# Optimization experiments

Measured on AMD Instinct MI355X. Metric: run time of the kernel, lower is better.

Reference implementation:

```python
import jax, jax.numpy as jnp
import numpy as np

N_X, N_M, E, D_IN, D_OUT = 200000, 50000, 600000, 128, 128
BN_EPS = 1e-5


def setup_inputs() -> dict:
    key = jax.random.key(0)
    ks = jax.random.split(key, 12)
    s = 0.02
    x_metrical = jax.random.normal(ks[0], (N_M, D_IN), dtype=jnp.float32)
    x = jax.random.normal(ks[1], (N_X, D_IN), dtype=jnp.float32)
    src = jax.random.randint(ks[2], (E,), 0, N_X)   # indexes x (note nodes)
    dst = jax.random.randint(ks[3], (E,), 0, N_M)   # indexes x_metrical
    edge_index = jnp.stack([src, dst], axis=0)
    batch = jnp.zeros((N_M,), dtype=jnp.int64 if jax.config.jax_enable_x64 else jnp.int32)
    return {
        "x_metrical": x_metrical,
        "x": x,
        "edge_index": edge_index,
        "batch": batch,
        "W_neigh": jax.random.normal(ks[4], (D_IN, D_IN), dtype=jnp.float32) * s,
        "b_neigh": jnp.zeros((D_IN,), dtype=jnp.float32),
        "W_l": jax.random.normal(ks[5], (D_IN, D_IN), dtype=jnp.float32) * s,  # SAGEConv lin_l (neighbors)
        "b_l": jnp.zeros((D_IN,), dtype=jnp.float32),
        "W_r": jax.random.normal(ks[6], (D_IN, D_IN), dtype=jnp.float32) * s,  # SAGEConv lin_r (root, no bias)
        "W_out": jax.random.normal(ks[7], (D_OUT, 3 * D_IN), dtype=jnp.float32) * s,
        "b_out": jnp.zeros((D_OUT,), dtype=jnp.float32),
        "gamma": jnp.ones((D_OUT,), dtype=jnp.float32),
        "beta": jnp.zeros((D_OUT,), dtype=jnp.float32),
    }


def reference(x_metrical, x, edge_index, batch, W_neigh, b_neigh, W_l, b_l, W_r,
              W_out, b_out, gamma, beta):
    n_m = x_metrical.shape[0]
    n_x = x.shape[0]
    src, dst = edge_index[0], edge_index[1]

    # neigh linear on note features, scatter-add onto metrical nodes
    h_neigh = x @ W_neigh.T + b_neigh                          # [N_x, D]
    h_scatter = jax.ops.segment_sum(h_neigh[src], dst, num_segments=n_m)  # [N_m, D]

    # SAGEConv(aggr='add') over the chain seq_index (batch all-equal branch):
    # edge i -> i+1, so sum-aggregation = shift x_metrical down by one row.
    agg = jnp.concatenate(
        [jnp.zeros((1, x_metrical.shape[1]), dtype=x_metrical.dtype), x_metrical[:-1]],
        axis=0)
    h_seq = agg @ W_l.T + b_l + x_metrical @ W_r.T             # [N_m, D]

    # concat + output linear (activation = Identity)
    h = jnp.concatenate([h_scatter, x_metrical, h_seq], axis=1)  # [N_m, 3D]
    h = h @ W_out.T + b_out                                      # [N_m, D_out]

    # BatchNorm1d (training-mode batch stats, biased variance); dropout = identity (eval)
    mean = jnp.mean(h, axis=0)
    var = jnp.mean((h - mean) ** 2, axis=0)
    h = (h - mean) * jax.lax.rsqrt(var + BN_EPS) * gamma + beta

    # final scatter-add back onto note nodes
    out = jax.ops.segment_sum(h[dst], src, num_segments=n_x)     # [N_x, D_out]
    return out
```

## Files before the change

kernel.cpp:

```cpp
#include <hip/hip_runtime.h>

#define D_IN 128
#define BN_EPS 1e-5f
#define BIN_SHIFT 8
#define MAXBIN 1024

typedef __attribute__((ext_vector_type(8))) __bf16 bf16x8;
typedef __attribute__((ext_vector_type(8))) unsigned short ushort8;
typedef __attribute__((ext_vector_type(4))) float f32x4;
typedef unsigned short ushort_t;

__device__ inline ushort_t f2bf(float x) {
    union { float f; unsigned u; } c; c.f = x;
    unsigned r = (c.u + 0x7fffu + ((c.u >> 16) & 1u)) >> 16;
    return (ushort_t)r;
}
__device__ inline float bf2f(ushort_t x) {
    union { unsigned u; float f; } c; c.u = ((unsigned)x) << 16;
    return c.f;
}
__device__ inline float lof(unsigned v) {
    union { unsigned u; float f; } c; c.u = v << 16;
    return c.f;
}
__device__ inline float hif(unsigned v) {
    union { unsigned u; float f; } c; c.u = v & 0xffff0000u;
    return c.f;
}

__global__ void combine_weights_k(const float* __restrict__ Wn, const float* __restrict__ bn,
                                  const float* __restrict__ Wl, const float* __restrict__ bl,
                                  const float* __restrict__ Wr, const float* __restrict__ Wo,
                                  const float* __restrict__ bo,
                                  ushort_t* __restrict__ Wb, float* __restrict__ c1,
                                  float* __restrict__ c0,
                                  int* __restrict__ binCnt,
                                  const float* __restrict__ xm, ushort_t* __restrict__ xmb,
                                  int n8m) {
    int b = blockIdx.x;
    int j = threadIdx.x;
    if (b < 384) {
        int term = b >> 7;
        int k = b & 127;
        float acc = 0.f;
        if (term == 0) {
            for (int t = 0; t < 128; ++t) acc += Wo[j * 384 + t] * Wn[t * 128 + k];
        } else if (term == 1) {
            acc = Wo[j * 384 + 128 + k];
            for (int t = 0; t < 128; ++t) acc += Wo[j * 384 + 256 + t] * Wr[t * 128 + k];
        } else {
            for (int t = 0; t < 128; ++t) acc += Wo[j * 384 + 256 + t] * Wl[t * 128 + k];
        }
        Wb[term * 16384 + j * 128 + k] = f2bf(acc);
    } else if (b == 384) {
        float a1 = 0.f, a0 = bo[j];
        for (int t = 0; t < 128; ++t) {
            a1 += Wo[j * 384 + t] * bn[t];
            a0 += Wo[j * 384 + 256 + t] * bl[t];
        }
        c1[j] = a1;
        c0[j] = a0;
    } else if (b == 385) {
        for (int i = j; i < MAXBIN; i += 128) binCnt[i] = 0;
    } else {
        int i = (b - 386) * 128 + j;
        if (i < n8m) {
            float4 f0 = ((const float4*)xm)[i * 2];
            float4 f1 = ((const float4*)xm)[i * 2 + 1];
            ushort8 o;
            o[0] = f2bf(f0.x); o[1] = f2bf(f0.y); o[2] = f2bf(f0.z); o[3] = f2bf(f0.w);
            o[4] = f2bf(f1.x); o[5] = f2bf(f1.y); o[6] = f2bf(f1.z); o[7] = f2bf(f1.w);
            ((ushort8*)xmb)[i] = o;
        }
    }
}


__global__ __launch_bounds__(256) void bin_hist_k(const int* __restrict__ src,
                                                  const int* __restrict__ dst,
                                                  int* __restrict__ binCnt,
                                                  int nE, int nM, int nBin) {
    __shared__ int h[MAXBIN];
    int t = threadIdx.x;
    for (int i = t; i < nBin; i += 256) h[i] = 0;
    __syncthreads();
    int total = 2 * nE;
    int per = (total + gridDim.x - 1) / gridDim.x;
    int lo = blockIdx.x * per, hi = min(lo + per, total);
    for (int i = lo + t; i < hi; i += 256) {
        int key = (i < nE) ? dst[i] : (nM + src[i - nE]);
        atomicAdd(&h[key >> BIN_SHIFT], 1);
    }
    __syncthreads();
    for (int i = t; i < nBin; i += 256) {
        int v = h[i];
        if (v) atomicAdd(&binCnt[i], v);
    }
}

__global__ __launch_bounds__(1024) void bin_scan_k(const int* __restrict__ binCnt,
                                                   int* __restrict__ binBase,
                                                   int* __restrict__ binCursor,
                                                   int* __restrict__ offs,
                                                   int nBin, int nTot, int total2E) {
    __shared__ int sc[1024];
    int t = threadIdx.x;
    int v = (t < nBin) ? binCnt[t] : 0;
    sc[t] = v;
    __syncthreads();
    for (int off = 1; off < 1024; off <<= 1) {
        int a = (t >= off) ? sc[t - off] : 0;
        __syncthreads();
        sc[t] += a;
        __syncthreads();
    }
    int excl = sc[t] - v;
    if (t <= nBin) binBase[t] = excl;
    if (t < nBin) binCursor[t] = excl;
    if (t == nBin) offs[nTot] = total2E;
}

__global__ __launch_bounds__(256) void bin_scatter_k(const int* __restrict__ src,
                                                     const int* __restrict__ dst,
                                                     int* __restrict__ binCursor,
                                                     unsigned* __restrict__ binned,
                                                     int nE, int nM, int nBin) {
    __shared__ int h[MAXBIN];
    __shared__ int base[MAXBIN];
    int t = threadIdx.x;
    for (int i = t; i < nBin; i += 256) h[i] = 0;
    __syncthreads();
    int total = 2 * nE;
    int per = (total + gridDim.x - 1) / gridDim.x;
    int lo = blockIdx.x * per, hi = min(lo + per, total);
    for (int i = lo + t; i < hi; i += 256) {
        int key = (i < nE) ? dst[i] : (nM + src[i - nE]);
        atomicAdd(&h[key >> BIN_SHIFT], 1);
    }
    __syncthreads();
    for (int i = t; i < nBin; i += 256) {
        int c = h[i];
        base[i] = c ? atomicAdd(&binCursor[i], c) : 0;
        h[i] = 0;
    }
    __syncthreads();
    for (int i = lo + t; i < hi; i += 256) {
        int key, val;
        if (i < nE) { key = dst[i]; val = src[i]; }
        else        { key = nM + src[i - nE]; val = dst[i - nE]; }
        int b = key >> BIN_SHIFT;
        int p = base[b] + atomicAdd(&h[b], 1);
        binned[p] = ((unsigned)(key & ((1 << BIN_SHIFT) - 1)) << 20) | (unsigned)val;
    }
}

__global__ __launch_bounds__(256) void bucket_sort_k(const unsigned* __restrict__ binned,
                                                     const int* __restrict__ binBase,
                                                     int* __restrict__ offs,
                                                     int* __restrict__ list, int nTot) {
    __shared__ int hist[256];
    __shared__ int sc[256];
    __shared__ int cur[256];
    int b = blockIdx.x;
    int base = binBase[b], end = binBase[b + 1];
    int n = end - base;
    int t = threadIdx.x;
    hist[t] = 0;
    __syncthreads();
    for (int i = t; i < n; i += 256) atomicAdd(&hist[binned[base + i] >> 20], 1);
    __syncthreads();
    int v = hist[t];
    sc[t] = v;
    __syncthreads();
    for (int off = 1; off < 256; off <<= 1) {
        int a = (t >= off) ? sc[t - off] : 0;
        __syncthreads();
        sc[t] += a;
        __syncthreads();
    }
    int excl = sc[t] - v;
    int bucket = (b << BIN_SHIFT) + t;
    if (bucket < nTot) offs[bucket] = base + excl;
    cur[t] = excl;
    __syncthreads();
    for (int i = t; i < n; i += 256) {
        unsigned p = binned[base + i];
        int lb = p >> 20;
        int pos = atomicAdd(&cur[lb], 1);
        list[base + pos] = (int)(p & 0xFFFFFu);
    }
}


__global__ __launch_bounds__(256) void gather_xs_k(const float4* __restrict__ x4,
                                                   const int* __restrict__ offs,
                                                   const int* __restrict__ list,
                                                   uint2* __restrict__ XS4, int nM) {
    int m = blockIdx.x * 8 + (threadIdx.x >> 5);
    if (m >= nM) return;
    int l = threadIdx.x & 31;
    int s = offs[m], e = offs[m + 1];
    float a0 = 0.f, a1 = 0.f, a2 = 0.f, a3 = 0.f;
    for (int s0 = s; s0 < e; s0 += 32) {
        int cnt = min(e - s0, 32);
        int r = (l < cnt) ? list[s0 + l] : 0;
        for (int i0 = 0; i0 < cnt; i0 += 8) {
            float4 v[8];
#pragma unroll
            for (int j = 0; j < 8; ++j) {
                int idx = i0 + j;
                int cl = idx < cnt ? idx : cnt - 1;
                int rr = __shfl(r, cl, 32);
                v[j] = x4[(size_t)rr * 32 + l];
            }
#pragma unroll
            for (int j = 0; j < 8; ++j) {
                if (i0 + j < cnt) {
                    a0 += v[j].x; a1 += v[j].y; a2 += v[j].z; a3 += v[j].w;
                }
            }
        }
    }
    uint2 o;
    o.x = (unsigned)f2bf(a0) | ((unsigned)f2bf(a1) << 16);
    o.y = (unsigned)f2bf(a2) | ((unsigned)f2bf(a3) << 16);
    XS4[(size_t)m * 32 + l] = o;
}

__global__ __launch_bounds__(256) void gemm_h_k(const ushort_t* __restrict__ XSb,
                                                const ushort_t* __restrict__ XMb,
                                                const ushort_t* __restrict__ Wb,
                                                const float* __restrict__ c1,
                                                const float* __restrict__ c0,
                                                const int* __restrict__ off,
                                                ushort_t* __restrict__ Hb,
                                                float* __restrict__ partS,
                                                float* __restrict__ partQ, int nM) {
    __shared__ float lds_s[4][128];
    __shared__ float lds_q[4][128];
    int wave = threadIdx.x >> 6, lane = threadIdx.x & 63;
    int m0 = blockIdx.x * 64 + wave * 16;
    int rl = lane & 15, kg = lane >> 4;
    f32x4 acc[8];
#pragma unroll
    for (int jt = 0; jt < 8; ++jt) acc[jt] = (f32x4){0.f, 0.f, 0.f, 0.f};
    int arow = m0 + rl;
    bool wave_live = (m0 < nM);
    if (wave_live) {
#pragma unroll
        for (int term = 0; term < 3; ++term) {
            const ushort_t* xp = (term == 0) ? XSb : XMb;
            int r2 = (term == 2) ? (arow - 1) : arow;
            bool valid = (r2 >= 0) && (arow < nM);
            const ushort_t* rp = xp + (size_t)r2 * D_IN + kg * 8;
            const ushort_t* wbase = Wb + term * 16384 + rl * 128 + kg * 8;
            bf16x8 a[4];
#pragma unroll
            for (int kc = 0; kc < 4; ++kc) {
                if (valid) {
                    a[kc] = *reinterpret_cast<const bf16x8*>(rp + kc * 32);
                } else {
#pragma unroll
                    for (int i = 0; i < 8; ++i) a[kc][i] = (__bf16)0.f;
                }
            }
#pragma unroll
            for (int kc = 0; kc < 4; ++kc) {
                bf16x8 bfr[8];
#pragma unroll
                for (int jt = 0; jt < 8; ++jt)
                    bfr[jt] = *reinterpret_cast<const bf16x8*>(wbase + jt * 2048 + kc * 32);
#pragma unroll
                for (int jt = 0; jt < 8; ++jt)
                    acc[jt] = __builtin_amdgcn_mfma_f32_16x16x32_bf16(a[kc], bfr[jt], acc[jt], 0, 0, 0);
            }
        }
    }
    float ssum[8], sq[8];
#pragma unroll
    for (int jt = 0; jt < 8; ++jt) { ssum[jt] = 0.f; sq[jt] = 0.f; }
    if (wave_live) {
        float cc1[8], cc0[8];
#pragma unroll
        for (int jt = 0; jt < 8; ++jt) { cc1[jt] = c1[jt * 16 + rl]; cc0[jt] = c0[jt * 16 + rl]; }
#pragma unroll
        for (int r = 0; r < 4; ++r) {
            int rowd = m0 + kg * 4 + r;
            if (rowd < nM) {
                float degv = (float)(off[rowd + 1] - off[rowd]);
                ushort_t* hp = Hb + (size_t)rowd * D_IN;
#pragma unroll
                for (int jt = 0; jt < 8; ++jt) {
                    float hv = acc[jt][r] + degv * cc1[jt] + cc0[jt];
                    hp[jt * 16 + rl] = f2bf(hv);
                    ssum[jt] += hv;
                    sq[jt] += hv * hv;
                }
            }
        }
    }
#pragma unroll
    for (int jt = 0; jt < 8; ++jt) {
        ssum[jt] += __shfl_xor(ssum[jt], 16, 64);
        ssum[jt] += __shfl_xor(ssum[jt], 32, 64);
        sq[jt]   += __shfl_xor(sq[jt], 16, 64);
        sq[jt]   += __shfl_xor(sq[jt], 32, 64);
    }
    if (lane < 16) {
#pragma unroll
        for (int jt = 0; jt < 8; ++jt) {
            lds_s[wave][jt * 16 + rl] = ssum[jt];
            lds_q[wave][jt * 16 + rl] = sq[jt];
        }
    }
    __syncthreads();
    if (threadIdx.x < 128) {
        int col = threadIdx.x;
        float s = lds_s[0][col] + lds_s[1][col] + lds_s[2][col] + lds_s[3][col];
        float q = lds_q[0][col] + lds_q[1][col] + lds_q[2][col] + lds_q[3][col];
        partS[(size_t)blockIdx.x * 128 + col] = s;
        partQ[(size_t)blockIdx.x * 128 + col] = q;
    }
}

__global__ __launch_bounds__(1024) void bn_reduce_k(const float* __restrict__ partS,
                                                    const float* __restrict__ partQ,
                                                    float* __restrict__ bnsum,
                                                    float* __restrict__ bnsq, int nB) {
    __shared__ float ls[8][128], lq[8][128];
    int col = threadIdx.x & 127, seg = threadIdx.x >> 7;
    float s = 0.f, q = 0.f;
    for (int b = seg; b < nB; b += 8) {
        s += partS[(size_t)b * 128 + col];
        q += partQ[(size_t)b * 128 + col];
    }
    ls[seg][col] = s;
    lq[seg][col] = q;
    __syncthreads();
    if (threadIdx.x < 128) {
        float S = 0.f, Q = 0.f;
#pragma unroll
        for (int i = 0; i < 8; ++i) { S += ls[i][col]; Q += lq[i][col]; }
        bnsum[col] = S;
        bnsq[col] = Q;
    }
}

__global__ __launch_bounds__(256) void gather_out_k(const uint2* __restrict__ H4,
                                                    const int* __restrict__ offs2,
                                                    const int* __restrict__ list,
                                                    const float* __restrict__ bnsum,
                                                    const float* __restrict__ bnsq,
                                                    const float* __restrict__ gamma,
                                                    const float* __restrict__ beta,
                                                    float* __restrict__ out,
                                                    int nX, int nM) {
    int n = blockIdx.x * 8 + (threadIdx.x >> 5);
    if (n >= nX) return;
    int l = threadIdx.x & 31;
    int s = offs2[n], e = offs2[n + 1];
    float a0 = 0.f, a1 = 0.f, a2 = 0.f, a3 = 0.f;
    for (int s0 = s; s0 < e; s0 += 32) {
        int cnt = min(e - s0, 32);
        int r = (l < cnt) ? list[s0 + l] : 0;
        for (int i0 = 0; i0 < cnt; i0 += 4) {
            uint2 v[4];
#pragma unroll
            for (int j = 0; j < 4; ++j) {
                int idx = i0 + j;
                int cl = idx < cnt ? idx : cnt - 1;
                int rr = __shfl(r, cl, 32);
                v[j] = H4[(size_t)rr * 32 + l];
            }
#pragma unroll
            for (int j = 0; j < 4; ++j) {
                if (i0 + j < cnt) {
                    a0 += lof(v[j].x); a1 += hif(v[j].x);
                    a2 += lof(v[j].y); a3 += hif(v[j].y);
                }
            }
        }
    }
    float4 s1 = ((const float4*)bnsum)[l];
    float4 s2 = ((const float4*)bnsq)[l];
    float4 g  = ((const float4*)gamma)[l];
    float4 be = ((const float4*)beta)[l];
    float inv = 1.0f / (float)nM;
    float cnt = (float)(e - s);
    f32x4 o;
    {
        float mean = s1.x * inv, var = s2.x * inv - mean * mean;
        float sc = g.x * rsqrtf(var + BN_EPS);
        o.x = sc * a0 + cnt * (be.x - mean * sc);
    }
    {
        float mean = s1.y * inv, var = s2.y * inv - mean * mean;
        float sc = g.y * rsqrtf(var + BN_EPS);
        o.y = sc * a1 + cnt * (be.y - mean * sc);
    }
    {
        float mean = s1.z * inv, var = s2.z * inv - mean * mean;
        float sc = g.z * rsqrtf(var + BN_EPS);
        o.z = sc * a2 + cnt * (be.z - mean * sc);
    }
    {
        float mean = s1.w * inv, var = s2.w * inv - mean * mean;
        float sc = g.w * rsqrtf(var + BN_EPS);
        o.w = sc * a3 + cnt * (be.w - mean * sc);
    }
    __builtin_nontemporal_store(o, (f32x4*)(out + (size_t)n * 128 + l * 4));
}

extern "C" void kernel_launch(void* const* d_in, const int* in_sizes, int n_in,
                              void* d_out, int out_size, void* d_ws, size_t ws_size,
                              hipStream_t stream) {
    const float* x_metrical = (const float*)d_in[0];
    const float* x          = (const float*)d_in[1];
    const int*   edge       = (const int*)d_in[2];
    const float* Wn    = (const float*)d_in[4];
    const float* bn    = (const float*)d_in[5];
    const float* Wl    = (const float*)d_in[6];
    const float* bl    = (const float*)d_in[7];
    const float* Wr    = (const float*)d_in[8];
    const float* Wo    = (const float*)d_in[9];
    const float* bo    = (const float*)d_in[10];
    const float* gamma = (const float*)d_in[11];
    const float* beta  = (const float*)d_in[12];
    float* out = (float*)d_out;

    int nM = in_sizes[0] / D_IN;
    int nX = in_sizes[1] / D_IN;
    int nE = in_sizes[2] / 2;
    int nTot = nM + nX;
    int nBin = (nTot + 255) >> BIN_SHIFT;
    int nBlkGemm = (nM + 63) / 64;
    const int* src = edge;
    const int* dst = edge + nE;

    char* ws = (char*)d_ws;
    size_t o = 0;
    auto alloc = [&](size_t bytes) -> void* {
        void* p = ws + o;
        o = (o + bytes + 255) & ~(size_t)255;
        return p;
    };
    ushort_t* Wb        = (ushort_t*)alloc((size_t)3 * 128 * 128 * 2);
    float*    c1        = (float*)alloc(512);
    float*    c0        = (float*)alloc(512);
    float*    bnsum     = (float*)alloc(512);
    float*    bnsq      = (float*)alloc(512);
    int*      binCnt    = (int*)alloc(4096);
    int*      binBase   = (int*)alloc(4104);
    int*      binCursor = (int*)alloc(4096);
    float*    partS     = (float*)alloc((size_t)nBlkGemm * 128 * 4);
    float*    partQ     = (float*)alloc((size_t)nBlkGemm * 128 * 4);
    int*      offs      = (int*)alloc(((size_t)nTot + 1) * 4);
    int*      list      = (int*)alloc((size_t)2 * nE * 4);
    size_t unionSz = (size_t)2 * nE * 4;
    size_t xsSz = (size_t)nM * D_IN * 2;
    char* uregion = (char*)alloc(unionSz > xsSz ? unionSz : xsSz);
    unsigned* binned = (unsigned*)uregion;
    ushort_t* XSb    = (ushort_t*)uregion;
    ushort_t* xmb    = (ushort_t*)alloc((size_t)nM * D_IN * 2);
    ushort_t* Hb     = (ushort_t*)alloc((size_t)nM * D_IN * 2);

    int n8m = nM * D_IN / 8;
    int nBlkComb = 386 + (n8m + 127) / 128;
    combine_weights_k<<<nBlkComb, 128, 0, stream>>>(Wn, bn, Wl, bl, Wr, Wo, bo, Wb, c1, c0,
                                                    binCnt, x_metrical, xmb, n8m);
    bin_hist_k<<<256, 256, 0, stream>>>(src, dst, binCnt, nE, nM, nBin);
    bin_scan_k<<<1, 1024, 0, stream>>>(binCnt, binBase, binCursor, offs, nBin, nTot, 2 * nE);
    bin_scatter_k<<<256, 256, 0, stream>>>(src, dst, binCursor, binned, nE, nM, nBin);
    bucket_sort_k<<<nBin, 256, 0, stream>>>(binned, binBase, offs, list, nTot);
    gather_xs_k<<<(nM + 7) / 8, 256, 0, stream>>>((const float4*)x, offs, list,
                                                  (uint2*)XSb, nM);
    gemm_h_k<<<nBlkGemm, 256, 0, stream>>>(XSb, xmb, Wb, c1, c0, offs, Hb,
                                           partS, partQ, nM);
    bn_reduce_k<<<1, 1024, 0, stream>>>(partS, partQ, bnsum, bnsq, nBlkGemm);
    gather_out_k<<<(nX + 7) / 8, 256, 0, stream>>>((const uint2*)Hb, offs + nM, list,
                                                   bnsum, bnsq, gamma, beta,
                                                   out, nX, nM);
}
```

Before: 232.8 us.

## Fuse histogram into preprocessing kernel and gather from bf16 copy of x

The edge-key histogram now runs inside the preprocessing kernel as per-block partial histograms, which bin_scan sums. This removes the separate histogram launch and the global atomics, and drops the binCnt zeroing dependency. The preprocessing kernel also converts all of x (200k x 128) to bf16, so the random-access gather reads 8 bytes per lane instead of 16. The cost is a full extra read and write pass over x (about 100 MB of traffic) and a bin_scan that loops over 512 partial rows. It also rounds x to bf16 before summation, which changes precision.

```diff
diff --git a/kernel.cpp b/kernel.cpp
--- a/kernel.cpp
+++ b/kernel.cpp
@@ -4,6 +4,7 @@
 #define BN_EPS 1e-5f
 #define BIN_SHIFT 8
 #define MAXBIN 1024
+#define NHB 512
 
 typedef __attribute__((ext_vector_type(8))) __bf16 bf16x8;
 typedef __attribute__((ext_vector_type(8))) unsigned short ushort8;
@@ -15,10 +16,6 @@
     unsigned r = (c.u + 0x7fffu + ((c.u >> 16) & 1u)) >> 16;
     return (ushort_t)r;
 }
-__device__ inline float bf2f(ushort_t x) {
-    union { unsigned u; float f; } c; c.u = ((unsigned)x) << 16;
-    return c.f;
-}
 __device__ inline float lof(unsigned v) {
     union { unsigned u; float f; } c; c.u = v << 16;
     return c.f;
@@ -28,20 +25,36 @@
     return c.f;
 }
 
-__global__ void combine_weights_k(const float* __restrict__ Wn, const float* __restrict__ bn,
-                                  const float* __restrict__ Wl, const float* __restrict__ bl,
-                                  const float* __restrict__ Wr, const float* __restrict__ Wo,
-                                  const float* __restrict__ bo,
-                                  ushort_t* __restrict__ Wb, float* __restrict__ c1,
-                                  float* __restrict__ c0,
-                                  int* __restrict__ binCnt,
-                                  const float* __restrict__ xm, ushort_t* __restrict__ xmb,
-                                  int n8m) {
+__global__ __launch_bounds__(128) void fused_pre_k(
+        const float* __restrict__ Wn, const float* __restrict__ bn,
+        const float* __restrict__ Wl, const float* __restrict__ bl,
+        const float* __restrict__ Wr, const float* __restrict__ Wo,
+        const float* __restrict__ bo,
+        ushort_t* __restrict__ Wb, float* __restrict__ c1, float* __restrict__ c0,
+        const int* __restrict__ src, const int* __restrict__ dst,
+        int* __restrict__ partHist,
+        const float* __restrict__ x, ushort_t* __restrict__ xb, int n8x, int nBlkX,
+        const float* __restrict__ xm, ushort_t* __restrict__ xmb, int n8m,
+        int nE, int nM, int nBin) {
+    __shared__ int h[MAXBIN];
     int b = blockIdx.x;
     int j = threadIdx.x;
-    if (b < 384) {
-        int term = b >> 7;
-        int k = b & 127;
+    if (b < NHB) {
+        for (int i = j; i < nBin; i += 128) h[i] = 0;
+        __syncthreads();
+        int total = 2 * nE;
+        int per = (total + NHB - 1) / NHB;
+        int lo = b * per, hi = min(lo + per, total);
+        for (int i = lo + j; i < hi; i += 128) {
+            int key = (i < nE) ? dst[i] : (nM + src[i - nE]);
+            atomicAdd(&h[key >> BIN_SHIFT], 1);
+        }
+        __syncthreads();
+        for (int i = j; i < nBin; i += 128) partHist[b * MAXBIN + i] = h[i];
+    } else if (b < NHB + 384) {
+        int bb = b - NHB;
+        int term = bb >> 7;
+        int k = bb & 127;
         float acc = 0.f;
         if (term == 0) {
             for (int t = 0; t < 128; ++t) acc += Wo[j * 384 + t] * Wn[t * 128 + k];
@@ -52,7 +65,7 @@
             for (int t = 0; t < 128; ++t) acc += Wo[j * 384 + 256 + t] * Wl[t * 128 + k];
         }
         Wb[term * 16384 + j * 128 + k] = f2bf(acc);
-    } else if (b == 384) {
+    } else if (b == NHB + 384) {
         float a1 = 0.f, a0 = bo[j];
         for (int t = 0; t < 128; ++t) {
             a1 += Wo[j * 384 + t] * bn[t];
@@ -60,52 +73,40 @@
         }
         c1[j] = a1;
         c0[j] = a0;
-    } else if (b == 385) {
-        for (int i = j; i < MAXBIN; i += 128) binCnt[i] = 0;
     } else {
-        int i = (b - 386) * 128 + j;
-        if (i < n8m) {
-            float4 f0 = ((const float4*)xm)[i * 2];
-            float4 f1 = ((const float4*)xm)[i * 2 + 1];
-            ushort8 o;
-            o[0] = f2bf(f0.x); o[1] = f2bf(f0.y); o[2] = f2bf(f0.z); o[3] = f2bf(f0.w);
-            o[4] = f2bf(f1.x); o[5] = f2bf(f1.y); o[6] = f2bf(f1.z); o[7] = f2bf(f1.w);
-            ((ushort8*)xmb)[i] = o;
-        }
-    }
-}
-
-
-__global__ __launch_bounds__(256) void bin_hist_k(const int* __restrict__ src,
-                                                  const int* __restrict__ dst,
-                                                  int* __restrict__ binCnt,
-                                                  int nE, int nM, int nBin) {
-    __shared__ int h[MAXBIN];
-    int t = threadIdx.x;
-    for (int i = t; i < nBin; i += 256) h[i] = 0;
-    __syncthreads();
-    int total = 2 * nE;
-    int per = (total + gridDim.x - 1) / gridDim.x;
-    int lo = blockIdx.x * per, hi = min(lo + per, total);
-    for (int i = lo + t; i < hi; i += 256) {
-        int key = (i < nE) ? dst[i] : (nM + src[i - nE]);
-        atomicAdd(&h[key >> BIN_SHIFT], 1);
-    }
-    __syncthreads();
-    for (int i = t; i < nBin; i += 256) {
-        int v = h[i];
-        if (v) atomicAdd(&binCnt[i], v);
-    }
-}
-
-__global__ __launch_bounds__(1024) void bin_scan_k(const int* __restrict__ binCnt,
+        int bb = b - (NHB + 385);
+        const float* in; ushort_t* out; int i;
+        if (bb < nBlkX) {
+            i = bb * 128 + j;
+            if (i >= n8x) return;
+            in = x; out = xb;
+        } else {
+            i = (bb - nBlkX) * 128 + j;
+            if (i >= n8m) return;
+            in = xm; out = xmb;
+        }
+        float4 f0 = ((const float4*)in)[i * 2];
+        float4 f1 = ((const float4*)in)[i * 2 + 1];
+        ushort8 o;
+        o[0] = f2bf(f0.x); o[1] = f2bf(f0.y); o[2] = f2bf(f0.z); o[3] = f2bf(f0.w);
+        o[4] = f2bf(f1.x); o[5] = f2bf(f1.y); o[6] = f2bf(f1.z); o[7] = f2bf(f1.w);
+        ((ushort8*)out)[i] = o;
+    }
+}
+
+
+__global__ __launch_bounds__(1024) void bin_scan_k(const int* __restrict__ partHist,
                                                    int* __restrict__ binBase,
                                                    int* __restrict__ binCursor,
                                                    int* __restrict__ offs,
                                                    int nBin, int nTot, int total2E) {
     __shared__ int sc[1024];
     int t = threadIdx.x;
-    int v = (t < nBin) ? binCnt[t] : 0;
+    int v = 0;
+    if (t < nBin) {
+#pragma unroll 8
+        for (int r = 0; r < NHB; ++r) v += partHist[r * MAXBIN + t];
+    }
     sc[t] = v;
     __syncthreads();
     for (int off = 1; off < 1024; off <<= 1) {
@@ -192,7 +193,7 @@
 }
 
 
-__global__ __launch_bounds__(256) void gather_xs_k(const float4* __restrict__ x4,
+__global__ __launch_bounds__(256) void gather_xs_k(const uint2* __restrict__ x4,
                                                    const int* __restrict__ offs,
                                                    const int* __restrict__ list,
                                                    uint2* __restrict__ XS4, int nM) {
@@ -205,7 +206,7 @@
         int cnt = min(e - s0, 32);
         int r = (l < cnt) ? list[s0 + l] : 0;
         for (int i0 = 0; i0 < cnt; i0 += 8) {
-            float4 v[8];
+            uint2 v[8];
 #pragma unroll
             for (int j = 0; j < 8; ++j) {
                 int idx = i0 + j;
@@ -216,7 +217,8 @@
 #pragma unroll
             for (int j = 0; j < 8; ++j) {
                 if (i0 + j < cnt) {
-                    a0 += v[j].x; a1 += v[j].y; a2 += v[j].z; a3 += v[j].w;
+                    a0 += lof(v[j].x); a1 += hif(v[j].x);
+                    a2 += lof(v[j].y); a3 += hif(v[j].y);
                 }
             }
         }
@@ -449,7 +451,7 @@
     float*    c0        = (float*)alloc(512);
     float*    bnsum     = (float*)alloc(512);
     float*    bnsq      = (float*)alloc(512);
-    int*      binCnt    = (int*)alloc(4096);
+    int*      partHist  = (int*)alloc((size_t)NHB * MAXBIN * 4);
     int*      binBase   = (int*)alloc(4104);
     int*      binCursor = (int*)alloc(4096);
     float*    partS     = (float*)alloc((size_t)nBlkGemm * 128 * 4);
@@ -462,17 +464,23 @@
     unsigned* binned = (unsigned*)uregion;
     ushort_t* XSb    = (ushort_t*)uregion;
     ushort_t* xmb    = (ushort_t*)alloc((size_t)nM * D_IN * 2);
+    ushort_t* xb     = (ushort_t*)alloc((size_t)nX * D_IN * 2);
     ushort_t* Hb     = (ushort_t*)alloc((size_t)nM * D_IN * 2);
 
+    int n8x = nX * D_IN / 8;
     int n8m = nM * D_IN / 8;
-    int nBlkComb = 386 + (n8m + 127) / 128;
-    combine_weights_k<<<nBlkComb, 128, 0, stream>>>(Wn, bn, Wl, bl, Wr, Wo, bo, Wb, c1, c0,
-                                                    binCnt, x_metrical, xmb, n8m);
-    bin_hist_k<<<256, 256, 0, stream>>>(src, dst, binCnt, nE, nM, nBin);
-    bin_scan_k<<<1, 1024, 0, stream>>>(binCnt, binBase, binCursor, offs, nBin, nTot, 2 * nE);
+    int nBlkX = (n8x + 127) / 128;
+    int nBlkM = (n8m + 127) / 128;
+    int nBlkPre = NHB + 385 + nBlkX + nBlkM;
+    fused_pre_k<<<nBlkPre, 128, 0, stream>>>(Wn, bn, Wl, bl, Wr, Wo, bo, Wb, c1, c0,
+                                             src, dst, partHist,
+                                             x, xb, n8x, nBlkX,
+                                             x_metrical, xmb, n8m,
+                                             nE, nM, nBin);
+    bin_scan_k<<<1, 1024, 0, stream>>>(partHist, binBase, binCursor, offs, nBin, nTot, 2 * nE);
     bin_scatter_k<<<256, 256, 0, stream>>>(src, dst, binCursor, binned, nE, nM, nBin);
     bucket_sort_k<<<nBin, 256, 0, stream>>>(binned, binBase, offs, list, nTot);
-    gather_xs_k<<<(nM + 7) / 8, 256, 0, stream>>>((const float4*)x, offs, list,
+    gather_xs_k<<<(nM + 7) / 8, 256, 0, stream>>>((const uint2*)xb, offs, list,
                                                   (uint2*)XSb, nM);
     gemm_h_k<<<nBlkGemm, 256, 0, stream>>>(XSb, xmb, Wb, c1, c0, offs, Hb,
                                            partS, partQ, nM);
```

New measurement: 241.9 us. +3.9%, slower.
